# Optimization experiments

Hardware: AMD Instinct MI355X
Metric: run time of the kernel (lower is better)

## Reference

```python
import jax, jax.numpy as jnp
import numpy as np

N = 10000
E = 160000
EMB = 10
ITERS = 3


def _linear_params(key, fan_in, fan_out):
    kw, kb = jax.random.split(key)
    # xavier-normal-ish init for the weight, small uniform for bias (as torch Linear default scale)
    w = jax.random.normal(kw, (fan_in, fan_out), dtype=jnp.float32) * np.float32(np.sqrt(2.0 / (fan_in + fan_out)))
    b = jax.random.uniform(kb, (fan_out,), dtype=jnp.float32, minval=-0.1, maxval=0.1)
    return w, b


def setup_inputs() -> dict:
    key = jax.random.key(0)
    ks = jax.random.split(key, 10)
    features = jax.random.normal(ks[0], (N,), dtype=jnp.float32)
    weights = jax.random.uniform(ks[1], (E,), dtype=jnp.float32)
    adjacency = jax.random.uniform(ks[2], (N, N), dtype=jnp.float32)
    ws_w, ws_b = _linear_params(ks[3], 1, EMB)          # w_selected
    wnp_w, wnp_b = _linear_params(ks[4], EMB, EMB)      # w_nbpriors
    wnw_w, wnw_b = _linear_params(ks[5], EMB, EMB)      # w_nbweights
    wew_w, wew_b = _linear_params(ks[6], 1, EMB)        # w_nbweights_ew
    wqr_w, wqr_b = _linear_params(ks[7], 2 * EMB, 1)    # w_q_reduc
    wqa_w, wqa_b = _linear_params(ks[8], EMB, EMB)      # w_q_allembed
    wqact_w, wqact_b = _linear_params(ks[9], EMB, EMB)  # w_q_action
    return {
        "features": features, "weights": weights, "adjacency": adjacency,
        "ws_w": ws_w, "ws_b": ws_b,
        "wnp_w": wnp_w, "wnp_b": wnp_b,
        "wnw_w": wnw_w, "wnw_b": wnw_b,
        "wew_w": wew_w, "wew_b": wew_b,
        "wqr_w": wqr_w, "wqr_b": wqr_b,
        "wqa_w": wqa_w, "wqa_b": wqa_b,
        "wqact_w": wqact_w, "wqact_b": wqact_b,
    }


def reference(features, weights, adjacency,
              ws_w, ws_b, wnp_w, wnp_b, wnw_w, wnw_b, wew_w, wew_b,
              wqr_w, wqr_b, wqa_w, wqa_b, wqact_w, wqact_b):
    n = adjacency.shape[0]
    # v_selected = w_selected(features[:, None])  -> (N, EMB)
    v_selected = features[:, None] @ ws_w + ws_b
    # edge weight embedding, summed over edges -> single (EMB,) vector
    edge_emb = jax.nn.relu(weights[:, None] @ wew_w + wew_b)  # (E, EMB)
    v_weights = jnp.sum(edge_emb, axis=0) @ wnw_w + wnw_b     # (EMB,)

    embeddings = jnp.zeros((n, EMB), dtype=features.dtype)
    for _ in range(ITERS):  # small fixed iteration count
        v_priors = (adjacency @ embeddings) @ wnp_w + wnp_b   # (N, EMB)
        embeddings = jax.nn.relu(v_selected + v_weights + v_priors)

    sumembed = jnp.sum(embeddings, axis=0) @ wqa_w + wqa_b    # (EMB,)
    peract = embeddings @ wqact_w + wqact_b                   # (N, EMB)
    q_in = jnp.concatenate([jnp.broadcast_to(sumembed[None, :], (n, EMB)), peract], axis=1)
    q_vals = (q_in @ wqr_w + wqr_b)[:, 0]                     # (N,)
    return q_vals, embeddings
```

## Files before the change

kernel.cpp:

```cpp
#include <hip/hip_runtime.h>

#define N_NODES 10000
#define EMB 10
#define NCHUNK 2500
#define ROWS 4

typedef float f32x4 __attribute__((ext_vector_type(4)));

#define WS_SEDGE 0
#define WS_SSUM  16
#define WS_EMBT  64

__global__ void k_edge_sum(const float* __restrict__ w, int E,
                           const float* __restrict__ wew_w,
                           const float* __restrict__ wew_b,
                           float* __restrict__ sEdge) {
    __shared__ float red[4][EMB];
    float a[EMB], b[EMB], acc[EMB];
#pragma unroll
    for (int j = 0; j < EMB; ++j) { a[j] = wew_w[j]; b[j] = wew_b[j]; acc[j] = 0.f; }
    for (int e = blockIdx.x * blockDim.x + threadIdx.x; e < E; e += gridDim.x * blockDim.x) {
        float we = w[e];
#pragma unroll
        for (int j = 0; j < EMB; ++j) acc[j] += fmaxf(we * a[j] + b[j], 0.f);
    }
#pragma unroll
    for (int m = 1; m < 64; m <<= 1)
#pragma unroll
        for (int j = 0; j < EMB; ++j) acc[j] += __shfl_xor(acc[j], m, 64);
    int wave = threadIdx.x >> 6, lane = threadIdx.x & 63;
    if (lane == 0)
#pragma unroll
        for (int j = 0; j < EMB; ++j) red[wave][j] = acc[j];
    __syncthreads();
    if (threadIdx.x < EMB)
        atomicAdd(&sEdge[threadIdx.x],
                  red[0][threadIdx.x] + red[1][threadIdx.x] + red[2][threadIdx.x] + red[3][threadIdx.x]);
}

template <bool FIRST>
__global__ __launch_bounds__(256) void k_iter(
    const float* __restrict__ A, const float* __restrict__ embT_in,
    const float* __restrict__ f, const float* __restrict__ ws_w,
    const float* __restrict__ ws_b, const float* __restrict__ wnp_w,
    const float* __restrict__ wnp_b, const float* __restrict__ wnw_w,
    const float* __restrict__ wnw_b, const float* __restrict__ sEdge,
    float* __restrict__ embT_out, float* __restrict__ emb_out,
    float* __restrict__ ssum) {
    const int tid  = threadIdx.x;
    const int wave = tid >> 6;
    const int lane = tid & 63;
    const int bid  = FIRST ? blockIdx.x : (gridDim.x - 1 - blockIdx.x);
    const int r0   = bid * ROWS;

    __shared__ float s_cb2[EMB];
    if (tid < EMB) {
        int j = tid;
        float v = wnw_b[j];
#pragma unroll
        for (int k = 0; k < EMB; ++k) v += sEdge[k] * wnw_w[k * EMB + j];
        s_cb2[j] = v + ws_b[j] + wnp_b[j];
    }
    __syncthreads();
    float cb2[EMB], wsw[EMB];
#pragma unroll
    for (int j = 0; j < EMB; ++j) { cb2[j] = s_cb2[j]; wsw[j] = ws_w[j]; }

    float acc[ROWS][EMB] = {};

    const f32x4* A0 = (const f32x4*)(A + (size_t)(r0 + 0) * N_NODES);
    const f32x4* A1 = (const f32x4*)(A + (size_t)(r0 + 1) * N_NODES);
    const f32x4* A2 = (const f32x4*)(A + (size_t)(r0 + 2) * N_NODES);
    const f32x4* A3 = (const f32x4*)(A + (size_t)(r0 + 3) * N_NODES);
    const f32x4* F4 = (const f32x4*)f;

#define BODY(c)                                                                     \
    {                                                                               \
        f32x4 a0, a1, a2, a3;                                                       \
        if (FIRST) {                                                                \
            a0 = A0[c]; a1 = A1[c]; a2 = A2[c]; a3 = A3[c];                         \
        } else {                                                                    \
            a0 = __builtin_nontemporal_load(A0 + (c));                              \
            a1 = __builtin_nontemporal_load(A1 + (c));                              \
            a2 = __builtin_nontemporal_load(A2 + (c));                              \
            a3 = __builtin_nontemporal_load(A3 + (c));                              \
        }                                                                           \
        f32x4 f4;                                                                   \
        if (FIRST) f4 = F4[c];                                                      \
        _Pragma("unroll")                                                           \
        for (int j = 0; j < EMB; ++j) {                                             \
            f32x4 e;                                                               \
            if (FIRST) {                                                            \
                e.x = fmaxf(f4.x * wsw[j] + cb2[j], 0.f);                           \
                e.y = fmaxf(f4.y * wsw[j] + cb2[j], 0.f);                           \
                e.z = fmaxf(f4.z * wsw[j] + cb2[j], 0.f);                           \
                e.w = fmaxf(f4.w * wsw[j] + cb2[j], 0.f);                           \
            } else {                                                                \
                e = ((const f32x4*)(embT_in + (size_t)j * N_NODES))[c];             \
            }                                                                       \
            acc[0][j] += a0.x * e.x + a0.y * e.y + a0.z * e.z + a0.w * e.w;         \
            acc[1][j] += a1.x * e.x + a1.y * e.y + a1.z * e.z + a1.w * e.w;         \
            acc[2][j] += a2.x * e.x + a2.y * e.y + a2.z * e.z + a2.w * e.w;         \
            acc[3][j] += a3.x * e.x + a3.y * e.y + a3.z * e.z + a3.w * e.w;         \
        }                                                                           \
    }

#pragma unroll 1
    for (int s = 0; s < 9; ++s) { int c = s * 256 + tid; BODY(c) }
    if (tid < NCHUNK - 9 * 256) { int c = 9 * 256 + tid; BODY(c) }
#undef BODY

#pragma unroll
    for (int m = 1; m < 64; m <<= 1)
#pragma unroll
        for (int r = 0; r < ROWS; ++r)
#pragma unroll
            for (int j = 0; j < EMB; ++j) acc[r][j] += __shfl_xor(acc[r][j], m, 64);

    __shared__ float part[4][ROWS * EMB];
    __shared__ float colp[ROWS * EMB];
    if (lane == 0)
#pragma unroll
        for (int r = 0; r < ROWS; ++r)
#pragma unroll
            for (int j = 0; j < EMB; ++j) part[wave][r * EMB + j] = acc[r][j];
    __syncthreads();

    if (tid < ROWS * EMB) {
        int r = tid / EMB, j = tid % EMB;
        float v = 0.f;
#pragma unroll
        for (int k = 0; k < EMB; ++k) {
            float yk = part[0][r * EMB + k] + part[1][r * EMB + k] +
                       part[2][r * EMB + k] + part[3][r * EMB + k];
            v += yk * wnp_w[k * EMB + j];
        }
        int i = r0 + r;
        v = fmaxf(f[i] * wsw[j] + cb2[j] + v, 0.f);
        if (FIRST) {
            embT_out[(size_t)j * N_NODES + i] = v;
        } else {
            emb_out[(size_t)i * EMB + j] = v;
            colp[tid] = v;
        }
    }
    if (!FIRST) {
        __syncthreads();
        if (tid < EMB)
            atomicAdd(&ssum[tid],
                      colp[tid] + colp[EMB + tid] + colp[2 * EMB + tid] + colp[3 * EMB + tid]);
    }
}

__global__ void k_out(const float* __restrict__ embRM, const float* __restrict__ ssum,
                      const float* __restrict__ wqa_w, const float* __restrict__ wqa_b,
                      const float* __restrict__ wqr_w, const float* __restrict__ wqr_b,
                      const float* __restrict__ wqact_w, const float* __restrict__ wqact_b,
                      float* __restrict__ q_out) {
    __shared__ float s_qvec[EMB];
    __shared__ float s_qc;
    int t = threadIdx.x;
    if (t == 0) {
        float qc = wqr_b[0];
        for (int tt = 0; tt < EMB; ++tt) {
            float se = wqa_b[tt];
            for (int k = 0; k < EMB; ++k) se += ssum[k] * wqa_w[k * EMB + tt];
            qc += se * wqr_w[tt] + wqact_b[tt] * wqr_w[EMB + tt];
        }
        s_qc = qc;
    }
    if (t < EMB) {
        float qv = 0.f;
#pragma unroll
        for (int j = 0; j < EMB; ++j) qv += wqact_w[t * EMB + j] * wqr_w[EMB + j];
        s_qvec[t] = qv;
    }
    __syncthreads();
    int i = blockIdx.x * blockDim.x + t;
    if (i < N_NODES) {
        float q = s_qc;
#pragma unroll
        for (int j = 0; j < EMB; ++j) q += embRM[(size_t)i * EMB + j] * s_qvec[j];
        q_out[i] = q;
    }
}

extern "C" void kernel_launch(void* const* d_in, const int* in_sizes, int n_in,
                              void* d_out, int out_size, void* d_ws, size_t ws_size,
                              hipStream_t stream) {
    (void)n_in; (void)out_size; (void)ws_size;
    const float* f      = (const float*)d_in[0];
    const float* w      = (const float*)d_in[1];
    const float* A      = (const float*)d_in[2];
    const float* ws_w   = (const float*)d_in[3];
    const float* ws_b   = (const float*)d_in[4];
    const float* wnp_w  = (const float*)d_in[5];
    const float* wnp_b  = (const float*)d_in[6];
    const float* wnw_w  = (const float*)d_in[7];
    const float* wnw_b  = (const float*)d_in[8];
    const float* wew_w  = (const float*)d_in[9];
    const float* wew_b  = (const float*)d_in[10];
    const float* wqr_w  = (const float*)d_in[11];
    const float* wqr_b  = (const float*)d_in[12];
    const float* wqa_w  = (const float*)d_in[13];
    const float* wqa_b  = (const float*)d_in[14];
    const float* wqact_w = (const float*)d_in[15];
    const float* wqact_b = (const float*)d_in[16];
    float* ws  = (float*)d_ws;
    float* out = (float*)d_out;
    const int E = in_sizes[1];

    float* outEmb = out + N_NODES;

    hipMemsetAsync(ws, 0, 64 * sizeof(float), stream);
    k_edge_sum<<<256, 256, 0, stream>>>(w, E, wew_w, wew_b, ws + WS_SEDGE);
    k_iter<true><<<N_NODES / ROWS, 256, 0, stream>>>(
        A, nullptr, f, ws_w, ws_b, wnp_w, wnp_b, wnw_w, wnw_b, ws + WS_SEDGE,
        ws + WS_EMBT, nullptr, nullptr);
    k_iter<false><<<N_NODES / ROWS, 256, 0, stream>>>(
        A, ws + WS_EMBT, f, ws_w, ws_b, wnp_w, wnp_b, wnw_w, wnw_b, ws + WS_SEDGE,
        nullptr, outEmb, ws + WS_SSUM);
    k_out<<<(N_NODES + 255) / 256, 256, 0, stream>>>(outEmb, ws + WS_SSUM,
                                                     wqa_w, wqa_b, wqr_w, wqr_b,
                                                     wqact_w, wqact_b, out);
}
```

Baseline: 680.5 us.

## Reverse column traversal in second pass and fuse per-node Q into iteration

The second adjacency pass previously ran its blocks in reverse order and used nontemporal loads. It now keeps the normal block order, uses plain loads, and walks each row's column chunks backwards, so the tail of A left in the large cache by the first pass is read first. The per-node Q dot product moves into the second iteration kernel, and a small follow-up kernel adds the global scalar term, so embeddings are no longer re-read. Reuse depends on how much of the 400MB matrix stays cache-resident and on how the scheduler orders blocks.

```diff
diff --git a/kernel.cpp b/kernel.cpp
--- a/kernel.cpp
+++ b/kernel.cpp
@@ -45,21 +45,28 @@
     const float* __restrict__ ws_b, const float* __restrict__ wnp_w,
     const float* __restrict__ wnp_b, const float* __restrict__ wnw_w,
     const float* __restrict__ wnw_b, const float* __restrict__ sEdge,
+    const float* __restrict__ wqr_w, const float* __restrict__ wqact_w,
     float* __restrict__ embT_out, float* __restrict__ emb_out,
-    float* __restrict__ ssum) {
+    float* __restrict__ ssum, float* __restrict__ q_out) {
     const int tid  = threadIdx.x;
     const int wave = tid >> 6;
     const int lane = tid & 63;
-    const int bid  = FIRST ? blockIdx.x : (gridDim.x - 1 - blockIdx.x);
-    const int r0   = bid * ROWS;
+    const int r0   = blockIdx.x * ROWS;
 
     __shared__ float s_cb2[EMB];
+    __shared__ float s_qvec[EMB];
     if (tid < EMB) {
         int j = tid;
         float v = wnw_b[j];
 #pragma unroll
         for (int k = 0; k < EMB; ++k) v += sEdge[k] * wnw_w[k * EMB + j];
         s_cb2[j] = v + ws_b[j] + wnp_b[j];
+        if (!FIRST) {
+            float qv = 0.f;
+#pragma unroll
+            for (int k = 0; k < EMB; ++k) qv += wqact_w[j * EMB + k] * wqr_w[EMB + k];
+            s_qvec[j] = qv;
+        }
     }
     __syncthreads();
     float cb2[EMB], wsw[EMB];
@@ -76,20 +83,12 @@
 
 #define BODY(c)                                                                     \
     {                                                                               \
-        f32x4 a0, a1, a2, a3;                                                       \
-        if (FIRST) {                                                                \
-            a0 = A0[c]; a1 = A1[c]; a2 = A2[c]; a3 = A3[c];                         \
-        } else {                                                                    \
-            a0 = __builtin_nontemporal_load(A0 + (c));                              \
-            a1 = __builtin_nontemporal_load(A1 + (c));                              \
-            a2 = __builtin_nontemporal_load(A2 + (c));                              \
-            a3 = __builtin_nontemporal_load(A3 + (c));                              \
-        }                                                                           \
+        f32x4 a0 = A0[c], a1 = A1[c], a2 = A2[c], a3 = A3[c];                       \
         f32x4 f4;                                                                   \
         if (FIRST) f4 = F4[c];                                                      \
         _Pragma("unroll")                                                           \
         for (int j = 0; j < EMB; ++j) {                                             \
-            f32x4 e;                                                               \
+            f32x4 e;                                                                \
             if (FIRST) {                                                            \
                 e.x = fmaxf(f4.x * wsw[j] + cb2[j], 0.f);                           \
                 e.y = fmaxf(f4.y * wsw[j] + cb2[j], 0.f);                           \
@@ -105,9 +104,17 @@
         }                                                                           \
     }
 
+    if (!FIRST) {
+        if (tid < NCHUNK - 9 * 256) { int c = 9 * 256 + tid; BODY(c) }
+    }
 #pragma unroll 1
-    for (int s = 0; s < 9; ++s) { int c = s * 256 + tid; BODY(c) }
-    if (tid < NCHUNK - 9 * 256) { int c = 9 * 256 + tid; BODY(c) }
+    for (int s = 0; s < 9; ++s) {
+        int c = (FIRST ? s : (8 - s)) * 256 + tid;
+        BODY(c)
+    }
+    if (FIRST) {
+        if (tid < NCHUNK - 9 * 256) { int c = 9 * 256 + tid; BODY(c) }
+    }
 #undef BODY
 
 #pragma unroll
@@ -149,40 +156,33 @@
         if (tid < EMB)
             atomicAdd(&ssum[tid],
                       colp[tid] + colp[EMB + tid] + colp[2 * EMB + tid] + colp[3 * EMB + tid]);
-    }
-}
-
-__global__ void k_out(const float* __restrict__ embRM, const float* __restrict__ ssum,
-                      const float* __restrict__ wqa_w, const float* __restrict__ wqa_b,
-                      const float* __restrict__ wqr_w, const float* __restrict__ wqr_b,
-                      const float* __restrict__ wqact_w, const float* __restrict__ wqact_b,
-                      float* __restrict__ q_out) {
-    __shared__ float s_qvec[EMB];
+        if (tid < ROWS) {
+            float q = 0.f;
+#pragma unroll
+            for (int j = 0; j < EMB; ++j) q += colp[tid * EMB + j] * s_qvec[j];
+            q_out[r0 + tid] = q;
+        }
+    }
+}
+
+__global__ void k_qc(const float* __restrict__ ssum,
+                     const float* __restrict__ wqa_w, const float* __restrict__ wqa_b,
+                     const float* __restrict__ wqr_w, const float* __restrict__ wqr_b,
+                     const float* __restrict__ wqact_b,
+                     float* __restrict__ q_out) {
     __shared__ float s_qc;
-    int t = threadIdx.x;
-    if (t == 0) {
+    if (threadIdx.x == 0) {
         float qc = wqr_b[0];
-        for (int tt = 0; tt < EMB; ++tt) {
-            float se = wqa_b[tt];
-            for (int k = 0; k < EMB; ++k) se += ssum[k] * wqa_w[k * EMB + tt];
-            qc += se * wqr_w[tt] + wqact_b[tt] * wqr_w[EMB + tt];
+        for (int t = 0; t < EMB; ++t) {
+            float se = wqa_b[t];
+            for (int k = 0; k < EMB; ++k) se += ssum[k] * wqa_w[k * EMB + t];
+            qc += se * wqr_w[t] + wqact_b[t] * wqr_w[EMB + t];
         }
         s_qc = qc;
     }
-    if (t < EMB) {
-        float qv = 0.f;
-#pragma unroll
-        for (int j = 0; j < EMB; ++j) qv += wqact_w[t * EMB + j] * wqr_w[EMB + j];
-        s_qvec[t] = qv;
-    }
-    __syncthreads();
-    int i = blockIdx.x * blockDim.x + t;
-    if (i < N_NODES) {
-        float q = s_qc;
-#pragma unroll
-        for (int j = 0; j < EMB; ++j) q += embRM[(size_t)i * EMB + j] * s_qvec[j];
-        q_out[i] = q;
-    }
+    __syncthreads();
+    int i = blockIdx.x * blockDim.x + threadIdx.x;
+    if (i < N_NODES) q_out[i] += s_qc;
 }
 
 extern "C" void kernel_launch(void* const* d_in, const int* in_sizes, int n_in,
@@ -216,11 +216,10 @@
     k_edge_sum<<<256, 256, 0, stream>>>(w, E, wew_w, wew_b, ws + WS_SEDGE);
     k_iter<true><<<N_NODES / ROWS, 256, 0, stream>>>(
         A, nullptr, f, ws_w, ws_b, wnp_w, wnp_b, wnw_w, wnw_b, ws + WS_SEDGE,
-        ws + WS_EMBT, nullptr, nullptr);
+        nullptr, nullptr, ws + WS_EMBT, nullptr, nullptr, nullptr);
     k_iter<false><<<N_NODES / ROWS, 256, 0, stream>>>(
         A, ws + WS_EMBT, f, ws_w, ws_b, wnp_w, wnp_b, wnw_w, wnw_b, ws + WS_SEDGE,
-        nullptr, outEmb, ws + WS_SSUM);
-    k_out<<<(N_NODES + 255) / 256, 256, 0, stream>>>(outEmb, ws + WS_SSUM,
-                                                     wqa_w, wqa_b, wqr_w, wqr_b,
-                                                     wqact_w, wqact_b, out);
-}
+        wqr_w, wqact_w, nullptr, outEmb, ws + WS_SSUM, out);
+    k_qc<<<(N_NODES + 255) / 256, 256, 0, stream>>>(ws + WS_SSUM, wqa_w, wqa_b,
+                                                    wqr_w, wqr_b, wqact_b, out);
+}
```

New measurement: 682.6 us. Within noise of the previous version (+0.3%).
